# Optimization experiments

Measured on AMD Instinct MI355X. Metric: run time of the kernel, lower is better.

The kernel has to match this reference:

```python
import jax, jax.numpy as jnp
import numpy as np

LN_EPS = 1e-12  # default nn.LayerNorm eps used by the HF ViT config


def setup_inputs() -> dict:
    key = jax.random.key(0)
    ks = jax.random.split(key, 6)
    B, H, S, D = 2, 12, 197, 768
    Hd = D // H
    hidden_states = jax.random.normal(ks[0], (B, S, D), jnp.float32)
    # attention probs: softmax-normalized over last axis for realism
    logits = jax.random.normal(ks[1], (B, H, S, S), jnp.float32)
    attention_probs = jax.nn.softmax(logits, axis=-1)
    value_layer = jax.random.normal(ks[2], (B, H, S, Hd), jnp.float32)
    dense_weight = jax.random.normal(ks[3], (D, D), jnp.float32) * 0.02
    ln_weight = jax.random.uniform(ks[4], (D,), jnp.float32, 0.5, 1.5)
    pre_ln_states = jax.random.normal(ks[5], (B, S, D), jnp.float32)
    return {
        'hidden_states': hidden_states,
        'attention_probs': attention_probs,
        'value_layer': value_layer,
        'dense_weight': dense_weight,
        'ln_weight': ln_weight,
        'pre_ln_states': pre_ln_states,
    }


def _norm(x):
    return jnp.linalg.norm(x, axis=-1)


def _diag_bsd(x):
    # torch.diagonal(x, dim1=1, dim2=2).permute(0,2,1): (b,k,s,d)->(b,s,d)
    return jnp.transpose(jnp.diagonal(x, axis1=1, axis2=2), (0, 2, 1))


def reference(hidden_states, attention_probs, value_layer, dense_weight, ln_weight, pre_ln_states):
    B, S, D = hidden_states.shape
    H = attention_probs.shape[1]
    Hd = D // H
    # dense.weight.view(all_head, H, Hd)
    dw = dense_weight.reshape(D, H, Hd)
    transformed = jnp.einsum('bhsv,dhv->bhsd', value_layer, dw)          # (B,H,S,D)
    weighted = jnp.einsum('bhks,bhsd->bhksd', attention_probs, transformed)  # (B,H,S,S,D)
    weighted_norm = _norm(weighted)                                       # (B,H,S,S)
    summed = weighted.sum(axis=1)                                         # (B,S,S,D)
    summed_norm = _norm(summed)
    residual = jnp.einsum('sk,bsd->bskd', jnp.eye(S, dtype=hidden_states.dtype), hidden_states)
    residual_weighted = summed + residual                                 # (B,S,S,D)
    residual_weighted_norm = _norm(residual_weighted)
    # LayerNorm decomposition: variance from pre_ln_states, mean per-component
    mean = pre_ln_states.mean(-1, keepdims=True)                          # (B,S,1)
    var = ((pre_ln_states - mean) ** 2).mean(-1, keepdims=True)[:, :, None]  # (B,S,1,1)
    each_mean = residual_weighted.mean(-1, keepdims=True)
    normalized = (residual_weighted - each_mean) / jnp.sqrt(var + LN_EPS)
    post_ln = normalized * ln_weight                                      # (B,S,S,D)
    post_ln_norm = _norm(post_ln)
    # mixing ratios
    def mixing_ratio(x):
        preserving = _diag_bsd(x)
        mixing = x.sum(axis=2) - preserving
        pn, mn = _norm(preserving), _norm(mixing)
        return mn / (mn + pn)
    attn_mix = mixing_ratio(summed)
    attnres_mix = mixing_ratio(residual_weighted)
    attnresln_mix = mixing_ratio(post_ln)
    return (weighted_norm, summed_norm, residual_weighted_norm, post_ln_norm,
            post_ln, attn_mix, attnres_mix, attnresln_mix)
```

## Files before the change

kernel.cpp:

```cpp
#include <hip/hip_runtime.h>
#include <cstdint>

#define S_ 197
#define D_ 768
#define H_ 12
#define B_ 2
#define SS_ (S_*S_)

#define O_WN   0
#define O_SN   931416
#define O_RWN  1009034
#define O_PLNN 1086652
#define O_PLN  1164270
#define O_AM   60774894
#define O_ARM  60775288
#define O_ARLM 60775682

#define WS_WT   0
#define WS_T2   589824
#define WS_TN   4220928
#define WS_ACC  4225656
#define WS_SMU  4830840
#define WS_DIAG 4831628
#define WS_MUI  5134220

#define I_T 4
#define NIT 50
#define NC 2
#define JC 99

__device__ __forceinline__ float wred64(float v) {
#pragma unroll
  for (int off = 32; off > 0; off >>= 1) v += __shfl_xor(v, off);
  return v;
}

__device__ __forceinline__ void load12(const float* __restrict__ p, float t[12]) {
  const float4* q = (const float4*)p;
  float4 a = q[0], b = q[1], c = q[2];
  t[0]=a.x; t[1]=a.y; t[2]=a.z; t[3]=a.w;
  t[4]=b.x; t[5]=b.y; t[6]=b.z; t[7]=b.w;
  t[8]=c.x; t[9]=c.y; t[10]=c.z; t[11]=c.w;
}

__global__ __launch_bounds__(256) void kTranspose(const float* __restrict__ in,
                                                  float* __restrict__ outp) {
  __shared__ float tile[32][33];
  int x = blockIdx.x*32 + threadIdx.x;
  int y = blockIdx.y*32 + threadIdx.y;
#pragma unroll
  for (int k = 0; k < 32; k += 8) tile[threadIdx.y+k][threadIdx.x] = in[(y+k)*D_ + x];
  __syncthreads();
  x = blockIdx.y*32 + threadIdx.x;
  y = blockIdx.x*32 + threadIdx.y;
#pragma unroll
  for (int k = 0; k < 32; k += 8) outp[(y+k)*D_ + x] = tile[threadIdx.x][threadIdx.y+k];
}

__global__ __launch_bounds__(256) void kTransform(const float* __restrict__ V,
                                                  const float* __restrict__ Wt,
                                                  float* __restrict__ T2,
                                                  float* __restrict__ tnorm) {
  int blk = blockIdx.x;
  int st = blk % 13; int bh = blk / 13;
  int h = bh % H_; int b = bh / H_;
  int s0 = st*16; int ns = min(16, S_ - s0);
  __shared__ float vt[16*64];
  __shared__ float red[4][16];
  int t = threadIdx.x;
  const float* Vbase = V + ((size_t)bh*S_ + s0)*64;
  for (int e = t; e < ns*64; e += 256) vt[e] = Vbase[e];
  __syncthreads();
  float acc2[16];
#pragma unroll
  for (int s = 0; s < 16; s++) acc2[s] = 0.f;
  for (int g = 0; g < 3; g++) {
    int d = t + g*256;
    float acc[16];
#pragma unroll
    for (int s = 0; s < 16; s++) acc[s] = 0.f;
    const float* wp = Wt + (size_t)h*64*D_ + d;
#pragma unroll 4
    for (int v = 0; v < 64; v++) {
      float wv = wp[(size_t)v*D_];
#pragma unroll
      for (int s = 0; s < 16; s++) acc[s] = fmaf(vt[s*64+v], wv, acc[s]);
    }
    for (int s = 0; s < ns; s++) {
      T2[((size_t)(b*S_ + s0+s)*H_ + h)*D_ + d] = acc[s];
      acc2[s] = fmaf(acc[s], acc[s], acc2[s]);
    }
  }
  int lane = t & 63, wq = t >> 6;
#pragma unroll
  for (int s = 0; s < 16; s++) {
    float v = wred64(acc2[s]);
    if (lane == 0) red[wq][s] = v;
  }
  __syncthreads();
  if (t < ns) {
    float v = red[0][t] + red[1][t] + red[2][t] + red[3][t];
    tnorm[bh*S_ + s0 + t] = sqrtf(v);
  }
}

__global__ __launch_bounds__(256) void kWeightedNorm(const float* __restrict__ attn,
                                                     const float* __restrict__ tnorm,
                                                     float* __restrict__ outp) {
  int idx = blockIdx.x*256 + threadIdx.x;
  if (idx < B_*H_*SS_) {
    int bh = idx / SS_;
    int s = idx % S_;
    outp[O_WN + idx] = fabsf(attn[idx]) * tnorm[bh*S_ + s];
  }
}

__global__ __launch_bounds__(768) void kMain(const float* __restrict__ attn,
                                             const float* __restrict__ hs,
                                             const float* __restrict__ lnw,
                                             const float* __restrict__ preln,
                                             const float* __restrict__ T2,
                                             float* __restrict__ outp,
                                             float* __restrict__ wsAccS,
                                             float* __restrict__ wsSmu,
                                             float* __restrict__ wsDiagS,
                                             float* __restrict__ wsMui) {
  int blk = blockIdx.x;
  int c = blk % NC; int r = blk / NC;
  int it = r % NIT; int b = r / NIT;
  int i0 = it * I_T;
  int jc0 = c * JC;
  int jcE = min(jc0 + JC, S_);
  int jcW = jcE - jc0;
  int ni = min(I_T, S_ - i0);
  int tid = threadIdx.x;
  int lane = tid & 63, wv = tid >> 6;
  int dbase = lane * 12;

  __shared__ float ash[H_*I_T*JC];
  __shared__ float sAcc[I_T*D_];
  __shared__ float sSmu[12*I_T];

  int tot = H_*I_T*jcW;
  for (int e = tid; e < tot; e += 768) {
    int hh = e / (I_T*jcW); int rem = e - hh*(I_T*jcW);
    int ii = rem / jcW; int jj = rem - ii*jcW;
    int iG = i0 + ii;
    float v = 0.f;
    if (iG < S_) v = attn[((size_t)(b*H_ + hh)*S_ + iG)*S_ + (jc0 + jj)];
    ash[(hh*I_T + ii)*JC + jj] = v;
  }

  float w_[12];
  load12(lnw + dbase, w_);
  float w2s_l = 0.f;
#pragma unroll
  for (int m = 0; m < 12; m++) w2s_l = fmaf(w_[m], w_[m], w2s_l);
  float w2sum = wred64(w2s_l);

  float istd[I_T];
#pragma unroll
  for (int ii = 0; ii < I_T; ii++) {
    int iG = i0 + ii;
    istd[ii] = 0.f;
    if (iG < S_) {
      float x[12];
      load12(preln + (size_t)(b*S_ + iG)*D_ + dbase, x);
      float sx = 0.f, sx2 = 0.f;
#pragma unroll
      for (int m = 0; m < 12; m++) { sx += x[m]; sx2 = fmaf(x[m], x[m], sx2); }
      sx = wred64(sx); sx2 = wred64(sx2);
      float mu = sx * (1.0f/768.0f);
      float var = sx2 * (1.0f/768.0f) - mu*mu;
      istd[ii] = 1.0f / sqrtf(var + 1e-12f);
    }
  }

  float accS[I_T][12];
#pragma unroll
  for (int ii = 0; ii < I_T; ii++)
#pragma unroll
    for (int m = 0; m < 12; m++) accS[ii][m] = 0.f;
  float smu[I_T] = {0.f, 0.f, 0.f, 0.f};

  __syncthreads();

  for (int j = jc0 + wv; j < jcE; j += 12) {
    int jj = j - jc0;
    const float* tb = T2 + (size_t)(b*S_ + j)*H_*D_ + dbase;
    float s[I_T][12];
#pragma unroll
    for (int ii = 0; ii < I_T; ii++)
#pragma unroll
      for (int m = 0; m < 12; m++) s[ii][m] = 0.f;
#pragma unroll 2
    for (int h = 0; h < H_; h++) {
      float t[12];
      load12(tb + h*D_, t);
#pragma unroll
      for (int ii = 0; ii < I_T; ii++) {
        float ah = ash[(h*I_T + ii)*JC + jj];
#pragma unroll
        for (int m = 0; m < 12; m++) s[ii][m] = fmaf(ah, t[m], s[ii][m]);
      }
    }
#pragma unroll
    for (int ii = 0; ii < I_T; ii++) {
      int iG = i0 + ii;
      if (iG < S_) {
        bool isDiag = (j == iG);
        float rw[12];
        if (isDiag) {
          float hh[12];
          load12(hs + (size_t)(b*S_ + iG)*D_ + dbase, hh);
#pragma unroll
          for (int m = 0; m < 12; m++) rw[m] = s[ii][m] + hh[m];
        } else {
#pragma unroll
          for (int m = 0; m < 12; m++) rw[m] = s[ii][m];
        }
        float ls2 = 0.f, lrw = 0.f, lrw2 = 0.f, lrww2 = 0.f, lrw2w2 = 0.f;
#pragma unroll
        for (int m = 0; m < 12; m++) {
          ls2 = fmaf(s[ii][m], s[ii][m], ls2);
          lrw += rw[m];
          float t1 = rw[m] * w_[m];
          lrww2 = fmaf(t1, w_[m], lrww2);
          lrw2 = fmaf(rw[m], rw[m], lrw2);
          lrw2w2 = fmaf(t1, t1, lrw2w2);
        }
        ls2 = wred64(ls2); lrw = wred64(lrw); lrw2 = wred64(lrw2);
        lrww2 = wred64(lrww2); lrw2w2 = wred64(lrw2w2);
        float mu = lrw * (1.0f/768.0f);
        float q = fmaf(mu*mu, w2sum, fmaf(-2.0f*mu, lrww2, lrw2w2));
        float plnn = istd[ii] * sqrtf(fmaxf(q, 0.f));
        int oIdx = (b*S_ + iG)*S_ + j;
        if (lane == 0) {
          outp[O_SN + oIdx] = sqrtf(ls2);
          outp[O_RWN + oIdx] = sqrtf(lrw2);
          outp[O_PLNN + oIdx] = plnn;
        }
        float* po = outp + O_PLN + (size_t)oIdx*D_ + dbase;
        float2* po2 = (float2*)po;
        float a = istd[ii];
#pragma unroll
        for (int m = 0; m < 12; m += 2) {
          float p0 = (rw[m]   - mu) * a * w_[m];
          float p1 = (rw[m+1] - mu) * a * w_[m+1];
          po2[m>>1] = make_float2(p0, p1);
        }
#pragma unroll
        for (int m = 0; m < 12; m++) accS[ii][m] += s[ii][m];
        smu[ii] += mu;
        if (isDiag) {
          float4* dp = (float4*)(wsDiagS + (size_t)(b*S_ + iG)*D_ + dbase);
          dp[0] = make_float4(s[ii][0], s[ii][1], s[ii][2],  s[ii][3]);
          dp[1] = make_float4(s[ii][4], s[ii][5], s[ii][6],  s[ii][7]);
          dp[2] = make_float4(s[ii][8], s[ii][9], s[ii][10], s[ii][11]);
          if (lane == 0) wsMui[b*S_ + iG] = mu;
        }
      }
    }
  }

  if (lane == 0) {
#pragma unroll
    for (int ii = 0; ii < I_T; ii++) sSmu[wv*I_T + ii] = smu[ii];
  }
  for (int rr = 0; rr < 12; rr++) {
    __syncthreads();
    if (wv == rr) {
#pragma unroll
      for (int ii = 0; ii < I_T; ii++) {
        if (ii < ni) {
#pragma unroll
          for (int m = 0; m < 12; m++) {
            int a = ii*D_ + dbase + m;
            sAcc[a] = (rr == 0) ? accS[ii][m] : (sAcc[a] + accS[ii][m]);
          }
        }
      }
    }
  }
  __syncthreads();
  if (tid < ni*192) {
    int ii = tid / 192; int d4 = (tid % 192) * 4;
    float4 v = *(float4*)&sAcc[ii*D_ + d4];
    *(float4*)(wsAccS + (size_t)((b*S_ + i0 + ii)*NC + c)*D_ + d4) = v;
  }
  if (tid < ni) {
    float ss = 0.f;
#pragma unroll
    for (int wq = 0; wq < 12; wq++) ss += sSmu[wq*I_T + tid];
    wsSmu[(b*S_ + i0 + tid)*NC + c] = ss;
  }
}

__global__ __launch_bounds__(256) void kMixing(const float* __restrict__ wsAccS,
                                               const float* __restrict__ wsSmu,
                                               const float* __restrict__ wsDiagS,
                                               const float* __restrict__ wsMui,
                                               const float* __restrict__ hs,
                                               const float* __restrict__ lnw,
                                               float* __restrict__ outp) {
  int bi = blockIdx.x;
  int t = threadIdx.x;
  float Smu = wsSmu[bi*2] + wsSmu[bi*2 + 1];
  float mui = wsMui[bi];
  float dmu = Smu - mui;
  float mS = 0.f, pS = 0.f, pRW = 0.f, mP = 0.f, pP = 0.f;
#pragma unroll
  for (int g = 0; g < 3; g++) {
    int d = t + g*256;
    float acc = wsAccS[(size_t)(bi*2)*D_ + d] + wsAccS[(size_t)(bi*2 + 1)*D_ + d];
    float dg = wsDiagS[(size_t)bi*D_ + d];
    float h = hs[(size_t)bi*D_ + d];
    float w = lnw[d];
    float mix = acc - dg;
    mS = fmaf(mix, mix, mS);
    pS = fmaf(dg, dg, pS);
    float drw = dg + h;
    pRW = fmaf(drw, drw, pRW);
    float mp = w * (mix - dmu);
    mP = fmaf(mp, mp, mP);
    float dp = w * (drw - mui);
    pP = fmaf(dp, dp, pP);
  }
  __shared__ float red[4][5];
  int lane = t & 63, wv = t >> 6;
  mS = wred64(mS); pS = wred64(pS); pRW = wred64(pRW); mP = wred64(mP); pP = wred64(pP);
  if (lane == 0) { red[wv][0]=mS; red[wv][1]=pS; red[wv][2]=pRW; red[wv][3]=mP; red[wv][4]=pP; }
  __syncthreads();
  if (t == 0) {
    float a0=0,a1=0,a2=0,a3=0,a4=0;
#pragma unroll
    for (int k = 0; k < 4; k++) { a0+=red[k][0]; a1+=red[k][1]; a2+=red[k][2]; a3+=red[k][3]; a4+=red[k][4]; }
    float mn = sqrtf(a0), pn = sqrtf(a1);
    outp[O_AM + bi] = mn / (mn + pn);
    float pnrw = sqrtf(a2);
    outp[O_ARM + bi] = mn / (mn + pnrw);
    float mnp = sqrtf(a3), pnp = sqrtf(a4);
    outp[O_ARLM + bi] = mnp / (mnp + pnp);
  }
}

extern "C" void kernel_launch(void* const* d_in, const int* in_sizes, int n_in,
                              void* d_out, int out_size, void* d_ws, size_t ws_size,
                              hipStream_t stream) {
  const float* hs    = (const float*)d_in[0];
  const float* attn  = (const float*)d_in[1];
  const float* V     = (const float*)d_in[2];
  const float* W     = (const float*)d_in[3];
  const float* lnw   = (const float*)d_in[4];
  const float* preln = (const float*)d_in[5];
  float* out = (float*)d_out;
  float* ws  = (float*)d_ws;

  kTranspose<<<dim3(24,24), dim3(32,8), 0, stream>>>(W, ws + WS_WT);
  kTransform<<<dim3(24*13), dim3(256), 0, stream>>>(V, ws + WS_WT, ws + WS_T2, ws + WS_TN);
  kWeightedNorm<<<dim3((B_*H_*SS_ + 255)/256), dim3(256), 0, stream>>>(attn, ws + WS_TN, out);
  kMain<<<dim3(B_*NIT*NC), dim3(768), 0, stream>>>(attn, hs, lnw, preln, ws + WS_T2, out,
                                                   ws + WS_ACC, ws + WS_SMU, ws + WS_DIAG, ws + WS_MUI);
  kMixing<<<dim3(B_*S_), dim3(256), 0, stream>>>(ws + WS_ACC, ws + WS_SMU, ws + WS_DIAG, ws + WS_MUI,
                                                 hs, lnw, out);
}
```

Baseline: 383.7 us.

## Compute norms via per-token Gram matrices and split main kernel into stages

Replaces the fused main kernel with a Gram-matrix approach. For each (b,j), inner products between the 12 head vectors and against the LN weights and hidden state are precomputed once, so the per-(i,j) norms become small quadratic forms in the attention weights instead of 768-wide reductions. The post-LN tensor write moves to its own kernel that keeps T2 for one j in registers and loops over i. Column sums go to a separate accumulation kernel. This removes the warp-reduction-heavy per-pair work, at the cost of extra launches, rereading attn and T2, and possible numeric cancellation in the Gram formulation.

```diff
diff --git a/kernel.cpp b/kernel.cpp
--- a/kernel.cpp
+++ b/kernel.cpp
@@ -6,6 +6,7 @@
 #define H_ 12
 #define B_ 2
 #define SS_ (S_*S_)
+#define NBJ (B_*S_)
 
 #define O_WN   0
 #define O_SN   931416
@@ -16,31 +17,32 @@
 #define O_ARM  60775288
 #define O_ARLM 60775682
 
+#define KG    0
+#define KGW   78
+#define KU    156
+#define KUW   168
+#define KHD   180
+#define KHWD  192
+#define KHSUM 204
+#define KHS2  205
+#define KHW2S 206
+#define KHW22 207
+#define KTOT  208
+
+#define WS_ACC  0
 #define WS_WT   0
-#define WS_T2   589824
-#define WS_TN   4220928
-#define WS_ACC  4225656
-#define WS_SMU  4830840
-#define WS_DIAG 4831628
-#define WS_MUI  5134220
-
-#define I_T 4
-#define NIT 50
-#define NC 2
-#define JC 99
+#define WS_T2   1210368
+#define WS_TN   4841472
+#define WS_GW   4846200
+#define WS_IST  4928152
+#define WS_SMU  4928546
+#define WS_MUI  4928940
+#define WS_DIAG 4929334
 
 __device__ __forceinline__ float wred64(float v) {
 #pragma unroll
   for (int off = 32; off > 0; off >>= 1) v += __shfl_xor(v, off);
   return v;
-}
-
-__device__ __forceinline__ void load12(const float* __restrict__ p, float t[12]) {
-  const float4* q = (const float4*)p;
-  float4 a = q[0], b = q[1], c = q[2];
-  t[0]=a.x; t[1]=a.y; t[2]=a.z; t[3]=a.w;
-  t[4]=b.x; t[5]=b.y; t[6]=b.z; t[7]=b.w;
-  t[8]=c.x; t[9]=c.y; t[10]=c.z; t[11]=c.w;
 }
 
 __global__ __launch_bounds__(256) void kTranspose(const float* __restrict__ in,
@@ -115,205 +117,312 @@
   }
 }
 
-__global__ __launch_bounds__(768) void kMain(const float* __restrict__ attn,
+#define TP 772
+__global__ __launch_bounds__(256) void kGram(const float* __restrict__ T2,
                                              const float* __restrict__ hs,
                                              const float* __restrict__ lnw,
-                                             const float* __restrict__ preln,
+                                             float* __restrict__ gw) {
+  int bj = blockIdx.x;
+  int t = threadIdx.x;
+  __shared__ float tl[H_*TP];
+  __shared__ float hl[D_];
+  __shared__ float w2l[D_];
+  const float* tb = T2 + (size_t)bj*H_*D_;
+#pragma unroll
+  for (int h = 0; h < H_; h++)
+    for (int d = t; d < D_; d += 256) tl[h*TP + d] = tb[h*D_ + d];
+  for (int d = t; d < D_; d += 256) {
+    hl[d] = hs[(size_t)bj*D_ + d];
+    float w = lnw[d];
+    w2l[d] = w*w;
+  }
+  __syncthreads();
+  float r = 0.f;
+  if (t < 156) {
+    int p = (t < 78) ? t : (t - 78);
+    int h = 0; int pp = p;
+    while (pp >= H_ - h) { pp -= H_ - h; h++; }
+    int h2 = h + pp;
+    const float4* ra = (const float4*)&tl[h*TP];
+    const float4* rb = (const float4*)&tl[h2*TP];
+    if (t < 78) {
+      for (int q = 0; q < D_/4; q++) {
+        float4 a = ra[q], b = rb[q];
+        r = fmaf(a.x,b.x, fmaf(a.y,b.y, fmaf(a.z,b.z, fmaf(a.w,b.w, r))));
+      }
+    } else {
+      const float4* rw = (const float4*)w2l;
+      for (int q = 0; q < D_/4; q++) {
+        float4 a = ra[q], b = rb[q], w = rw[q];
+        r = fmaf(w.x*a.x,b.x, fmaf(w.y*a.y,b.y, fmaf(w.z*a.z,b.z, fmaf(w.w*a.w,b.w, r))));
+      }
+    }
+    if (h != h2) r *= 2.f;
+  } else if (t < 204) {
+    int k = t - 156;
+    int h = k % 12; int kind = k / 12;
+    const float4* ra = (const float4*)&tl[h*TP];
+    const float4* rw = (const float4*)w2l;
+    const float4* rh = (const float4*)hl;
+    for (int q = 0; q < D_/4; q++) {
+      float4 a = ra[q];
+      float4 m;
+      if (kind == 0)      m = make_float4(1.f,1.f,1.f,1.f);
+      else if (kind == 1) m = rw[q];
+      else if (kind == 2) m = rh[q];
+      else { float4 w = rw[q], hh = rh[q]; m = make_float4(w.x*hh.x, w.y*hh.y, w.z*hh.z, w.w*hh.w); }
+      r = fmaf(m.x,a.x, fmaf(m.y,a.y, fmaf(m.z,a.z, fmaf(m.w,a.w, r))));
+    }
+    if (kind == 0) r *= (1.0f/768.0f);
+  } else if (t < 208) {
+    int kind = t - 204;
+    const float4* rw = (const float4*)w2l;
+    const float4* rh = (const float4*)hl;
+    for (int q = 0; q < D_/4; q++) {
+      float4 hh = rh[q]; float4 w = rw[q];
+      float4 m;
+      if (kind == 0)      m = make_float4(1.f,1.f,1.f,1.f);
+      else if (kind == 1) m = hh;
+      else if (kind == 2) m = w;
+      else                m = make_float4(w.x*hh.x, w.y*hh.y, w.z*hh.z, w.w*hh.w);
+      r = fmaf(m.x,hh.x, fmaf(m.y,hh.y, fmaf(m.z,hh.z, fmaf(m.w,hh.w, r))));
+    }
+    if (kind == 0) r *= (1.0f/768.0f);
+  }
+  if (t < KTOT) gw[(size_t)t*NBJ + bj] = r;
+}
+
+__global__ __launch_bounds__(256) void kNorms(const float* __restrict__ attn,
+                                              const float* __restrict__ preln,
+                                              const float* __restrict__ lnw,
+                                              const float* __restrict__ gw,
+                                              float* __restrict__ outp,
+                                              float* __restrict__ wsIst,
+                                              float* __restrict__ wsSmu,
+                                              float* __restrict__ wsMui) {
+  int bi = blockIdx.x;
+  int b = bi / S_; int i = bi % S_;
+  int t = threadIdx.x;
+  int lane = t & 63, wq = t >> 6;
+  __shared__ float red[4][3];
+  __shared__ float sc[2];
+  __shared__ float redmu[4];
+  float sx=0.f, sx2=0.f, sw2=0.f;
+#pragma unroll
+  for (int g = 0; g < 3; g++) {
+    int d = t + g*256;
+    float x = preln[(size_t)bi*D_ + d];
+    sx += x; sx2 = fmaf(x,x,sx2);
+    float w = lnw[d];
+    sw2 = fmaf(w,w,sw2);
+  }
+  sx = wred64(sx); sx2 = wred64(sx2); sw2 = wred64(sw2);
+  if (lane==0){ red[wq][0]=sx; red[wq][1]=sx2; red[wq][2]=sw2; }
+  __syncthreads();
+  if (t==0) {
+    float a0=0,a1=0,a2=0;
+#pragma unroll
+    for (int k=0;k<4;k++){a0+=red[k][0];a1+=red[k][1];a2+=red[k][2];}
+    float mu = a0*(1.f/768.f);
+    float var = a1*(1.f/768.f) - mu*mu;
+    float istd = rsqrtf(var + 1e-12f);
+    sc[0]=istd; sc[1]=a2;
+    wsIst[bi]=istd;
+  }
+  __syncthreads();
+  float istd = sc[0], w2sum = sc[1];
+  int j = t;
+  float mu = 0.f;
+  if (j < S_) {
+    int bj = b*S_ + j;
+    float a[12];
+#pragma unroll
+    for (int h=0; h<12; h++)
+      a[h] = attn[(((size_t)(b*H_ + h))*S_ + i)*S_ + j];
+    float sg=0.f, sgw=0.f;
+    int k=0;
+#pragma unroll
+    for (int h=0; h<12; h++) {
+#pragma unroll
+      for (int h2=h; h2<12; h2++) {
+        float pp = a[h]*a[h2];
+        sg  = fmaf(pp, gw[(size_t)(KG+k)*NBJ + bj], sg);
+        sgw = fmaf(pp, gw[(size_t)(KGW+k)*NBJ + bj], sgw);
+        k++;
+      }
+    }
+    float mus=0.f, s1w=0.f;
+#pragma unroll
+    for (int h=0; h<12; h++) {
+      mus = fmaf(a[h], gw[(size_t)(KU+h)*NBJ + bj], mus);
+      s1w = fmaf(a[h], gw[(size_t)(KUW+h)*NBJ + bj], s1w);
+    }
+    float rw2 = sg, s2w = sgw;
+    mu = mus;
+    if (j == i) {
+      float hd=0.f, hwd=0.f;
+#pragma unroll
+      for (int h=0; h<12; h++) {
+        hd  = fmaf(a[h], gw[(size_t)(KHD+h)*NBJ + bj], hd);
+        hwd = fmaf(a[h], gw[(size_t)(KHWD+h)*NBJ + bj], hwd);
+      }
+      rw2 += 2.f*hd + gw[(size_t)KHS2*NBJ + bj];
+      s2w += 2.f*hwd + gw[(size_t)KHW22*NBJ + bj];
+      s1w += gw[(size_t)KHW2S*NBJ + bj];
+      mu  += gw[(size_t)KHSUM*NBJ + bj];
+      wsMui[bi] = mu;
+    }
+    float q = fmaf(mu*mu, w2sum, fmaf(-2.f*mu, s1w, s2w));
+    int oIdx = bi*S_ + j;
+    outp[O_SN  + oIdx] = sqrtf(fmaxf(sg,0.f));
+    outp[O_RWN + oIdx] = sqrtf(fmaxf(rw2,0.f));
+    outp[O_PLNN+ oIdx] = istd * sqrtf(fmaxf(q,0.f));
+  }
+  float m = wred64(mu);
+  if (lane==0) redmu[wq]=m;
+  __syncthreads();
+  if (t==0) wsSmu[bi] = redmu[0]+redmu[1]+redmu[2]+redmu[3];
+}
+
+__global__ __launch_bounds__(256) void kPostLN(const float* __restrict__ attn,
+                                               const float* __restrict__ hs,
+                                               const float* __restrict__ lnw,
+                                               const float* __restrict__ T2,
+                                               const float* __restrict__ gw,
+                                               const float* __restrict__ wsIst,
+                                               float* __restrict__ outp,
+                                               float* __restrict__ wsDiag) {
+  int blk = blockIdx.x;
+  int ih = blk & 1; int bj = blk >> 1;
+  int b = bj / S_; int j = bj % S_;
+  int i0 = ih * 99;
+  int ni = min(99, S_ - i0);
+  int t = threadIdx.x;
+  __shared__ float aL[99*12];
+  __shared__ float uL[13];
+  __shared__ float muL[99];
+  __shared__ float istL[99];
+  for (int e = t; e < ni*12; e += 256) {
+    int ii = e / 12; int h = e % 12;
+    aL[e] = attn[(((size_t)(b*H_+h))*S_ + (i0+ii))*S_ + j];
+  }
+  if (t < 12) uL[t] = gw[(size_t)(KU+t)*NBJ + bj];
+  if (t == 12) uL[12] = gw[(size_t)KHSUM*NBJ + bj];
+  if (t < ni) istL[t] = wsIst[b*S_ + i0 + t];
+  float t2r[12][3];
+  const float* tb = T2 + (size_t)bj*H_*D_;
+#pragma unroll
+  for (int h=0; h<12; h++)
+#pragma unroll
+    for (int g=0; g<3; g++) t2r[h][g] = tb[h*D_ + t + g*256];
+  float wv[3], hv[3];
+#pragma unroll
+  for (int g=0; g<3; g++) { wv[g] = lnw[t+g*256]; hv[g] = hs[(size_t)bj*D_ + t + g*256]; }
+  __syncthreads();
+  if (t < ni) {
+    float m = 0.f;
+#pragma unroll
+    for (int h=0; h<12; h++) m = fmaf(aL[t*12+h], uL[h], m);
+    if (i0 + t == j) m += uL[12];
+    muL[t] = m;
+  }
+  __syncthreads();
+  for (int ii = 0; ii < ni; ii++) {
+    int iG = i0 + ii;
+    const float4* ap = (const float4*)&aL[ii*12];
+    float4 a0 = ap[0], a1 = ap[1], a2 = ap[2];
+    float aa[12] = {a0.x,a0.y,a0.z,a0.w,a1.x,a1.y,a1.z,a1.w,a2.x,a2.y,a2.z,a2.w};
+    float mu = muL[ii], ist = istL[ii];
+    bool diag = (iG == j);
+    float* po = outp + O_PLN + ((size_t)(b*S_+iG)*S_ + j)*D_;
+#pragma unroll
+    for (int g=0; g<3; g++) {
+      float s = 0.f;
+#pragma unroll
+      for (int h=0; h<12; h++) s = fmaf(aa[h], t2r[h][g], s);
+      float rw = s;
+      if (diag) rw += hv[g];
+      po[t + g*256] = (rw - mu) * ist * wv[g];
+      if (diag) wsDiag[(size_t)bj*D_ + t + g*256] = s;
+    }
+  }
+}
+
+#define AIT 8
+#define ANC 4
+#define AJW 50
+__global__ __launch_bounds__(256) void kAccS(const float* __restrict__ attn,
                                              const float* __restrict__ T2,
-                                             float* __restrict__ outp,
-                                             float* __restrict__ wsAccS,
-                                             float* __restrict__ wsSmu,
-                                             float* __restrict__ wsDiagS,
-                                             float* __restrict__ wsMui) {
+                                             float* __restrict__ wsAcc) {
   int blk = blockIdx.x;
-  int c = blk % NC; int r = blk / NC;
-  int it = r % NIT; int b = r / NIT;
-  int i0 = it * I_T;
-  int jc0 = c * JC;
-  int jcE = min(jc0 + JC, S_);
-  int jcW = jcE - jc0;
-  int ni = min(I_T, S_ - i0);
-  int tid = threadIdx.x;
-  int lane = tid & 63, wv = tid >> 6;
-  int dbase = lane * 12;
-
-  __shared__ float ash[H_*I_T*JC];
-  __shared__ float sAcc[I_T*D_];
-  __shared__ float sSmu[12*I_T];
-
-  int tot = H_*I_T*jcW;
-  for (int e = tid; e < tot; e += 768) {
-    int hh = e / (I_T*jcW); int rem = e - hh*(I_T*jcW);
-    int ii = rem / jcW; int jj = rem - ii*jcW;
+  int c = blk & 3; int r = blk >> 2;
+  int it = r % 25; int b = r / 25;
+  int i0 = it * AIT;
+  int j0 = c * AJW;
+  int jw = min(AJW, S_ - j0);
+  int t = threadIdx.x;
+  __shared__ float aL[AJW*100];
+  for (int e = t; e < H_*AIT*jw; e += 256) {
+    int h = e / (AIT*jw); int rem = e % (AIT*jw);
+    int ii = rem / jw; int jj = rem % jw;
     int iG = i0 + ii;
     float v = 0.f;
-    if (iG < S_) v = attn[((size_t)(b*H_ + hh)*S_ + iG)*S_ + (jc0 + jj)];
-    ash[(hh*I_T + ii)*JC + jj] = v;
-  }
-
-  float w_[12];
-  load12(lnw + dbase, w_);
-  float w2s_l = 0.f;
-#pragma unroll
-  for (int m = 0; m < 12; m++) w2s_l = fmaf(w_[m], w_[m], w2s_l);
-  float w2sum = wred64(w2s_l);
-
-  float istd[I_T];
-#pragma unroll
-  for (int ii = 0; ii < I_T; ii++) {
-    int iG = i0 + ii;
-    istd[ii] = 0.f;
-    if (iG < S_) {
-      float x[12];
-      load12(preln + (size_t)(b*S_ + iG)*D_ + dbase, x);
-      float sx = 0.f, sx2 = 0.f;
-#pragma unroll
-      for (int m = 0; m < 12; m++) { sx += x[m]; sx2 = fmaf(x[m], x[m], sx2); }
-      sx = wred64(sx); sx2 = wred64(sx2);
-      float mu = sx * (1.0f/768.0f);
-      float var = sx2 * (1.0f/768.0f) - mu*mu;
-      istd[ii] = 1.0f / sqrtf(var + 1e-12f);
-    }
-  }
-
-  float accS[I_T][12];
-#pragma unroll
-  for (int ii = 0; ii < I_T; ii++)
-#pragma unroll
-    for (int m = 0; m < 12; m++) accS[ii][m] = 0.f;
-  float smu[I_T] = {0.f, 0.f, 0.f, 0.f};
-
-  __syncthreads();
-
-  for (int j = jc0 + wv; j < jcE; j += 12) {
-    int jj = j - jc0;
-    const float* tb = T2 + (size_t)(b*S_ + j)*H_*D_ + dbase;
-    float s[I_T][12];
-#pragma unroll
-    for (int ii = 0; ii < I_T; ii++)
-#pragma unroll
-      for (int m = 0; m < 12; m++) s[ii][m] = 0.f;
+    if (iG < S_) v = attn[(((size_t)(b*H_+h))*S_ + iG)*S_ + (j0+jj)];
+    aL[jj*100 + h*8 + ii] = v;
+  }
+  __syncthreads();
+  float acc[AIT][3];
+#pragma unroll
+  for (int ii=0; ii<AIT; ii++)
+#pragma unroll
+    for (int g=0; g<3; g++) acc[ii][g] = 0.f;
+  for (int jj = 0; jj < jw; jj++) {
+    const float* tb = T2 + ((size_t)(b*S_ + j0 + jj))*H_*D_;
 #pragma unroll 2
     for (int h = 0; h < H_; h++) {
-      float t[12];
-      load12(tb + h*D_, t);
-#pragma unroll
-      for (int ii = 0; ii < I_T; ii++) {
-        float ah = ash[(h*I_T + ii)*JC + jj];
-#pragma unroll
-        for (int m = 0; m < 12; m++) s[ii][m] = fmaf(ah, t[m], s[ii][m]);
-      }
-    }
-#pragma unroll
-    for (int ii = 0; ii < I_T; ii++) {
-      int iG = i0 + ii;
-      if (iG < S_) {
-        bool isDiag = (j == iG);
-        float rw[12];
-        if (isDiag) {
-          float hh[12];
-          load12(hs + (size_t)(b*S_ + iG)*D_ + dbase, hh);
-#pragma unroll
-          for (int m = 0; m < 12; m++) rw[m] = s[ii][m] + hh[m];
-        } else {
-#pragma unroll
-          for (int m = 0; m < 12; m++) rw[m] = s[ii][m];
-        }
-        float ls2 = 0.f, lrw = 0.f, lrw2 = 0.f, lrww2 = 0.f, lrw2w2 = 0.f;
-#pragma unroll
-        for (int m = 0; m < 12; m++) {
-          ls2 = fmaf(s[ii][m], s[ii][m], ls2);
-          lrw += rw[m];
-          float t1 = rw[m] * w_[m];
-          lrww2 = fmaf(t1, w_[m], lrww2);
-          lrw2 = fmaf(rw[m], rw[m], lrw2);
-          lrw2w2 = fmaf(t1, t1, lrw2w2);
-        }
-        ls2 = wred64(ls2); lrw = wred64(lrw); lrw2 = wred64(lrw2);
-        lrww2 = wred64(lrww2); lrw2w2 = wred64(lrw2w2);
-        float mu = lrw * (1.0f/768.0f);
-        float q = fmaf(mu*mu, w2sum, fmaf(-2.0f*mu, lrww2, lrw2w2));
-        float plnn = istd[ii] * sqrtf(fmaxf(q, 0.f));
-        int oIdx = (b*S_ + iG)*S_ + j;
-        if (lane == 0) {
-          outp[O_SN + oIdx] = sqrtf(ls2);
-          outp[O_RWN + oIdx] = sqrtf(lrw2);
-          outp[O_PLNN + oIdx] = plnn;
-        }
-        float* po = outp + O_PLN + (size_t)oIdx*D_ + dbase;
-        float2* po2 = (float2*)po;
-        float a = istd[ii];
-#pragma unroll
-        for (int m = 0; m < 12; m += 2) {
-          float p0 = (rw[m]   - mu) * a * w_[m];
-          float p1 = (rw[m+1] - mu) * a * w_[m+1];
-          po2[m>>1] = make_float2(p0, p1);
-        }
-#pragma unroll
-        for (int m = 0; m < 12; m++) accS[ii][m] += s[ii][m];
-        smu[ii] += mu;
-        if (isDiag) {
-          float4* dp = (float4*)(wsDiagS + (size_t)(b*S_ + iG)*D_ + dbase);
-          dp[0] = make_float4(s[ii][0], s[ii][1], s[ii][2],  s[ii][3]);
-          dp[1] = make_float4(s[ii][4], s[ii][5], s[ii][6],  s[ii][7]);
-          dp[2] = make_float4(s[ii][8], s[ii][9], s[ii][10], s[ii][11]);
-          if (lane == 0) wsMui[b*S_ + iG] = mu;
-        }
-      }
-    }
-  }
-
-  if (lane == 0) {
-#pragma unroll
-    for (int ii = 0; ii < I_T; ii++) sSmu[wv*I_T + ii] = smu[ii];
-  }
-  for (int rr = 0; rr < 12; rr++) {
-    __syncthreads();
-    if (wv == rr) {
-#pragma unroll
-      for (int ii = 0; ii < I_T; ii++) {
-        if (ii < ni) {
-#pragma unroll
-          for (int m = 0; m < 12; m++) {
-            int a = ii*D_ + dbase + m;
-            sAcc[a] = (rr == 0) ? accS[ii][m] : (sAcc[a] + accS[ii][m]);
-          }
-        }
-      }
-    }
-  }
-  __syncthreads();
-  if (tid < ni*192) {
-    int ii = tid / 192; int d4 = (tid % 192) * 4;
-    float4 v = *(float4*)&sAcc[ii*D_ + d4];
-    *(float4*)(wsAccS + (size_t)((b*S_ + i0 + ii)*NC + c)*D_ + d4) = v;
-  }
-  if (tid < ni) {
-    float ss = 0.f;
-#pragma unroll
-    for (int wq = 0; wq < 12; wq++) ss += sSmu[wq*I_T + tid];
-    wsSmu[(b*S_ + i0 + tid)*NC + c] = ss;
-  }
-}
-
-__global__ __launch_bounds__(256) void kMixing(const float* __restrict__ wsAccS,
+      float t2v[3];
+#pragma unroll
+      for (int g=0; g<3; g++) t2v[g] = tb[h*D_ + t + g*256];
+      const float4* ap = (const float4*)&aL[jj*100 + h*8];
+      float4 x = ap[0], y = ap[1];
+      float av[8] = {x.x,x.y,x.z,x.w,y.x,y.y,y.z,y.w};
+#pragma unroll
+      for (int ii=0; ii<8; ii++)
+#pragma unroll
+        for (int g=0; g<3; g++) acc[ii][g] = fmaf(av[ii], t2v[g], acc[ii][g]);
+    }
+  }
+#pragma unroll
+  for (int ii=0; ii<AIT; ii++) {
+    int iG = i0 + ii;
+    if (iG < S_) {
+#pragma unroll
+      for (int g=0; g<3; g++)
+        wsAcc[((size_t)(b*S_+iG)*ANC + c)*D_ + t + g*256] = acc[ii][g];
+    }
+  }
+}
+
+__global__ __launch_bounds__(256) void kMixing(const float* __restrict__ wsAcc,
                                                const float* __restrict__ wsSmu,
-                                               const float* __restrict__ wsDiagS,
+                                               const float* __restrict__ wsDiag,
                                                const float* __restrict__ wsMui,
                                                const float* __restrict__ hs,
                                                const float* __restrict__ lnw,
                                                float* __restrict__ outp) {
   int bi = blockIdx.x;
   int t = threadIdx.x;
-  float Smu = wsSmu[bi*2] + wsSmu[bi*2 + 1];
+  float Smu = wsSmu[bi];
   float mui = wsMui[bi];
   float dmu = Smu - mui;
   float mS = 0.f, pS = 0.f, pRW = 0.f, mP = 0.f, pP = 0.f;
 #pragma unroll
   for (int g = 0; g < 3; g++) {
     int d = t + g*256;
-    float acc = wsAccS[(size_t)(bi*2)*D_ + d] + wsAccS[(size_t)(bi*2 + 1)*D_ + d];
-    float dg = wsDiagS[(size_t)bi*D_ + d];
+    float acc = 0.f;
+#pragma unroll
+    for (int cc = 0; cc < ANC; cc++) acc += wsAcc[((size_t)bi*ANC + cc)*D_ + d];
+    float dg = wsDiag[(size_t)bi*D_ + d];
     float h = hs[(size_t)bi*D_ + d];
     float w = lnw[d];
     float mix = acc - dg;
@@ -359,8 +468,12 @@
   kTranspose<<<dim3(24,24), dim3(32,8), 0, stream>>>(W, ws + WS_WT);
   kTransform<<<dim3(24*13), dim3(256), 0, stream>>>(V, ws + WS_WT, ws + WS_T2, ws + WS_TN);
   kWeightedNorm<<<dim3((B_*H_*SS_ + 255)/256), dim3(256), 0, stream>>>(attn, ws + WS_TN, out);
-  kMain<<<dim3(B_*NIT*NC), dim3(768), 0, stream>>>(attn, hs, lnw, preln, ws + WS_T2, out,
-                                                   ws + WS_ACC, ws + WS_SMU, ws + WS_DIAG, ws + WS_MUI);
-  kMixing<<<dim3(B_*S_), dim3(256), 0, stream>>>(ws + WS_ACC, ws + WS_SMU, ws + WS_DIAG, ws + WS_MUI,
-                                                 hs, lnw, out);
-}
+  kGram<<<dim3(NBJ), dim3(256), 0, stream>>>(ws + WS_T2, hs, lnw, ws + WS_GW);
+  kNorms<<<dim3(NBJ), dim3(256), 0, stream>>>(attn, preln, lnw, ws + WS_GW, out,
+                                              ws + WS_IST, ws + WS_SMU, ws + WS_MUI);
+  kPostLN<<<dim3(NBJ*2), dim3(256), 0, stream>>>(attn, hs, lnw, ws + WS_T2, ws + WS_GW,
+                                                 ws + WS_IST, out, ws + WS_DIAG);
+  kAccS<<<dim3(200), dim3(256), 0, stream>>>(attn, ws + WS_T2, ws + WS_ACC);
+  kMixing<<<dim3(NBJ), dim3(256), 0, stream>>>(ws + WS_ACC, ws + WS_SMU, ws + WS_DIAG, ws + WS_MUI,
+                                               hs, lnw, out);
+}
```

New measurement: 520.6 us. +35.7%, slower.
